# Optimization experiments

Hardware: AMD Instinct MI355X
Metric: run time of the kernel (lower is better)

## Reference

```python
import jax, jax.numpy as jnp
import numpy as np

B, N, T, D, H, E = 2, 1024, 8, 128, 4, 8192
DH = D // H
NEG_SLOPE = 0.2  # GATv2Conv default negative_slope


def _ln(x, g, b):
    m = jnp.mean(x, -1, keepdims=True)
    v = jnp.mean((x - m) ** 2, -1, keepdims=True)
    return (x - m) * jax.lax.rsqrt(v + 1e-5) * g + b


def _forward(x, edge_index, gat_wl, gat_wr, gat_att, gat_b, in_w, in_b, out_w, out_b,
             ffn_w1, ffn_b1, ffn_w2, ffn_b2, fus_w, fus_b,
             lns_g, lns_b, lnt1_g, lnt1_b, lnt2_g, lnt2_b, lnf_g, lnf_b):
    # ---- spatial branch: GATv2, vectorized over (B, T) instead of python loops ----
    loops = jnp.arange(N)
    src = jnp.concatenate([edge_index[0], loops])  # j: message source (PyG adds self loops)
    dst = jnp.concatenate([edge_index[1], loops])  # i: aggregation target
    xl = jnp.einsum('bntd,de->bnte', x, gat_wl).reshape(B, N, T, H, D)
    xr = jnp.einsum('bntd,de->bnte', x, gat_wr).reshape(B, N, T, H, D)
    ml = xl[:, src]                                  # [B,Et,T,H,D]
    mr = xr[:, dst]
    e = jax.nn.leaky_relu(ml + mr, NEG_SLOPE)
    logits = jnp.einsum('bethd,hd->beth', e, gat_att)
    logits = jnp.moveaxis(logits, 1, 0)              # [Et,B,T,H]
    mx = jax.ops.segment_max(logits, dst, num_segments=N)
    p = jnp.exp(logits - mx[dst])                    # stable edge softmax per dst node
    ssum = jax.ops.segment_sum(p, dst, num_segments=N)
    alpha = p / ssum[dst]                            # [Et,B,T,H]
    msg = alpha[..., None] * jnp.moveaxis(ml, 1, 0)
    agg = jax.ops.segment_sum(msg, dst, num_segments=N)  # [N,B,T,H,D]
    x_sp = jnp.moveaxis(agg.mean(3), 0, 1) + gat_b   # concat=False -> head mean; [B,N,T,D]
    x_sp = _ln(x_sp, lns_g, lns_b)

    # ---- temporal branch: MHA + FFN, vectorized over all B*N nodes ----
    xt = x.reshape(B * N, T, D)
    qkv = xt @ in_w + in_b
    q, k, v = jnp.split(qkv, 3, axis=-1)
    q = q.reshape(B * N, T, H, DH)
    k = k.reshape(B * N, T, H, DH)
    v = v.reshape(B * N, T, H, DH)
    scores = jnp.einsum('bthd,bshd->bhts', q, k) / np.float32(np.sqrt(DH))
    attn = jax.nn.softmax(scores, -1)
    o = jnp.einsum('bhts,bshd->bthd', attn, v).reshape(B * N, T, D)
    o = o @ out_w + out_b
    x1 = _ln(xt + o, lnt1_g, lnt1_b)
    ffn = jax.nn.gelu(x1 @ ffn_w1 + ffn_b1, approximate=False) @ ffn_w2 + ffn_b2
    x_tp = _ln(x1 + ffn, lnt2_g, lnt2_b).reshape(B, N, T, D)

    # ---- gated fusion with residual ----
    g = jax.nn.sigmoid(jnp.concatenate([x_sp, x_tp], -1) @ fus_w + fus_b)
    return _ln(g * x_sp + (1.0 - g) * x_tp + x, lnf_g, lnf_b)


def setup_inputs() -> dict:
    key = jax.random.key(0)
    ks = jax.random.split(key, 12)
    s = 0.05
    f = jnp.float32
    return {
        'x': jax.random.normal(ks[0], (B, N, T, D), f),
        'edge_index': jax.random.randint(ks[1], (2, E), 0, N),
        'gat_wl': jax.random.normal(ks[2], (D, H * D), f) * s,
        'gat_wr': jax.random.normal(ks[3], (D, H * D), f) * s,
        'gat_att': jax.random.normal(ks[4], (H, D), f) * s,
        'gat_b': jnp.zeros((D,), f),
        'in_w': jax.random.normal(ks[5], (D, 3 * D), f) * s,
        'in_b': jnp.zeros((3 * D,), f),
        'out_w': jax.random.normal(ks[6], (D, D), f) * s,
        'out_b': jnp.zeros((D,), f),
        'ffn_w1': jax.random.normal(ks[7], (D, 4 * D), f) * s,
        'ffn_b1': jnp.zeros((4 * D,), f),
        'ffn_w2': jax.random.normal(ks[8], (4 * D, D), f) * s,
        'ffn_b2': jnp.zeros((D,), f),
        'fus_w': jax.random.normal(ks[9], (2 * D, D), f) * s,
        'fus_b': jnp.zeros((D,), f),
        'lns_g': jnp.ones((D,), f), 'lns_b': jnp.zeros((D,), f),
        'lnt1_g': jnp.ones((D,), f), 'lnt1_b': jnp.zeros((D,), f),
        'lnt2_g': jnp.ones((D,), f), 'lnt2_b': jnp.zeros((D,), f),
        'lnf_g': jnp.ones((D,), f), 'lnf_b': jnp.zeros((D,), f),
    }


def reference(x, edge_index, gat_wl, gat_wr, gat_att, gat_b, in_w, in_b, out_w, out_b,
              ffn_w1, ffn_b1, ffn_w2, ffn_b2, fus_w, fus_b,
              lns_g, lns_b, lnt1_g, lnt1_b, lnt2_g, lnt2_b, lnf_g, lnf_b):
    return _forward(x, edge_index, gat_wl, gat_wr, gat_att, gat_b, in_w, in_b, out_w, out_b,
                    ffn_w1, ffn_b1, ffn_w2, ffn_b2, fus_w, fus_b,
                    lns_g, lns_b, lnt1_g, lnt1_b, lnt2_g, lnt2_b, lnf_g, lnf_b)
```

## Files before the change

kernel.cpp:

```cpp
#include <hip/hip_runtime.h>
#include <math.h>

#define B_ 2
#define N_ 1024
#define T_ 8
#define D_ 128
#define H_ 4
#define E_ 8192
#define EN_ 9216
#define M_ 16384

typedef unsigned short u16;
using bf16x8 = __attribute__((ext_vector_type(8))) short;
using f32x4  = __attribute__((ext_vector_type(4))) float;

__device__ __forceinline__ float bf2f(unsigned int u) {
  return __uint_as_float(u << 16);
}
__device__ __forceinline__ u16 f2bf(float f) {
  unsigned int x = __float_as_uint(f);
  x += 0x7fffu + ((x >> 16) & 1u);
  return (u16)(x >> 16);
}
__device__ __forceinline__ void load8f(const u16* p, float* f) {
  uint4 u = *(const uint4*)p;
  f[0]=bf2f(u.x & 0xffffu); f[1]=bf2f(u.x >> 16);
  f[2]=bf2f(u.y & 0xffffu); f[3]=bf2f(u.y >> 16);
  f[4]=bf2f(u.z & 0xffffu); f[5]=bf2f(u.z >> 16);
  f[6]=bf2f(u.w & 0xffffu); f[7]=bf2f(u.w >> 16);
}
__device__ __forceinline__ void unpack8(uint4 u, float* f) {
  f[0]=bf2f(u.x & 0xffffu); f[1]=bf2f(u.x >> 16);
  f[2]=bf2f(u.y & 0xffffu); f[3]=bf2f(u.y >> 16);
  f[4]=bf2f(u.z & 0xffffu); f[5]=bf2f(u.z >> 16);
  f[6]=bf2f(u.w & 0xffffu); f[7]=bf2f(u.w >> 16);
}
__device__ __forceinline__ void gl2lds(const u16* g, u16* l) {
  __builtin_amdgcn_global_load_lds(
      (const __attribute__((address_space(1))) unsigned int*)(const void*)g,
      (__attribute__((address_space(3))) unsigned int*)(void*)l,
      16, 0, 0);
}

__device__ __forceinline__ size_t bt_row(int r) {
  return (size_t)(((r >> 13) << 3) | (r & 7)) * 1024 + ((r >> 3) & 1023);
}

__device__ __forceinline__ u16 conv_w_elem(int idx,
    const float* wl, const float* wr, const float* inw, const float* outw,
    const float* f1, const float* f2, const float* fw) {
  const float* src; int base, K, N;
  if      (idx < 65536)  { src = wl;   base = 0;      K = 128; N = 512; }
  else if (idx < 131072) { src = wr;   base = 65536;  K = 128; N = 512; }
  else if (idx < 180224) { src = inw;  base = 131072; K = 128; N = 384; }
  else if (idx < 196608) { src = outw; base = 180224; K = 128; N = 128; }
  else if (idx < 262144) { src = f1;   base = 196608; K = 128; N = 512; }
  else if (idx < 327680) { src = f2;   base = 262144; K = 512; N = 128; }
  else                   { src = fw;   base = 327680; K = 256; N = 128; }
  int o = idx - base;
  int n = o / K, k = o - n * K;
  return f2bf(src[k * N + n]);
}

__global__ __launch_bounds__(1024) void prep_csr_k(const float* __restrict__ x,
    const float* __restrict__ wl, const float* __restrict__ wr,
    const float* __restrict__ inw, const float* __restrict__ outw,
    const float* __restrict__ f1, const float* __restrict__ f2,
    const float* __restrict__ fw,
    u16* __restrict__ XB, u16* __restrict__ WB,
    const int* __restrict__ ei, int* __restrict__ offs, int* __restrict__ srcs) {
  __shared__ int cnt[N_];
  __shared__ int cur[N_];
  int bi = blockIdx.x;
  int tid = threadIdx.x;
  if (bi < 512) {
    int i = (bi * 1024 + tid) * 4;
    float4 v = *(const float4*)&x[i];
    u16 o[4] = {f2bf(v.x), f2bf(v.y), f2bf(v.z), f2bf(v.w)};
    *(ushort4*)&XB[i] = *(ushort4*)o;
    return;
  }
  if (bi < 600) {
    int base = (bi - 512) * 4096 + tid * 4;
#pragma unroll
    for (int j = 0; j < 4; ++j)
      WB[base + j] = conv_w_elem(base + j, wl, wr, inw, outw, f1, f2, fw);
    return;
  }
  cnt[tid] = 0;
  __syncthreads();
  for (int e = tid; e < EN_; e += 1024) {
    int d = (e < E_) ? ei[E_ + e] : (e - E_);
    atomicAdd(&cnt[d], 1);
  }
  __syncthreads();
  int mine = cnt[tid];
  for (int off = 1; off < 1024; off <<= 1) {
    int tv = (tid >= off) ? cnt[tid - off] : 0;
    __syncthreads();
    cnt[tid] += tv;
    __syncthreads();
  }
  int excl = cnt[tid] - mine;
  offs[tid] = excl;
  if (tid == 1023) offs[N_] = cnt[1023];
  cur[tid] = excl;
  __syncthreads();
  for (int e = tid; e < EN_; e += 1024) {
    int d = (e < E_) ? ei[E_ + e] : (e - E_);
    int s = (e < E_) ? ei[e] : (e - E_);
    int pos = atomicAdd(&cur[d], 1);
    srcs[pos] = s;
  }
}

__global__ __launch_bounds__(256) void proj_k(const u16* __restrict__ XB,
    const u16* __restrict__ WT1, const float* __restrict__ in_b,
    u16* __restrict__ XL, u16* __restrict__ XR, u16* __restrict__ QKV) {
  __shared__ u16 As[128 * 128];
  __shared__ u16 Bs[128 * 128];
  int bx = blockIdx.x, by = blockIdx.y;
  int tid = threadIdx.x;
  int lane = tid & 63, wid = tid >> 6;
  int lr = lane & 15, lk = lane >> 4;
  int wm = (wid >> 1) * 64, wn = (wid & 1) * 64;

#pragma unroll
  for (int kc = 0; kc < 4; ++kc) {
#pragma unroll
    for (int i = 0; i < 2; ++i) {
      int o = tid * 16 + i * 4096;
      int row = o >> 6;
      int col = (o >> 1) & 31;
      gl2lds(XB + (size_t)(by * 128 + row) * 128 + kc * 32 + col,
             (u16*)((char*)As + kc * 8192 + i * 4096 + wid * 1024));
      gl2lds(WT1 + (size_t)(bx * 128 + row) * 128 + kc * 32 + col,
             (u16*)((char*)Bs + kc * 8192 + i * 4096 + wid * 1024));
    }
  }
  __syncthreads();

  f32x4 acc[4][4] = {};
#pragma unroll
  for (int kc = 0; kc < 4; ++kc) {
    bf16x8 bf[4];
#pragma unroll
    for (int ni = 0; ni < 4; ++ni)
      bf[ni] = *(const bf16x8*)&Bs[kc * 4096 + (wn + ni * 16 + lr) * 32 + lk * 8];
#pragma unroll
    for (int mi = 0; mi < 4; ++mi) {
      bf16x8 af = *(const bf16x8*)&As[kc * 4096 + (wm + mi * 16 + lr) * 32 + lk * 8];
#pragma unroll
      for (int ni = 0; ni < 4; ++ni)
        acc[mi][ni] = __builtin_amdgcn_mfma_f32_16x16x32_bf16(af, bf[ni], acc[mi][ni], 0, 0, 0);
    }
  }

  u16* Cb; int ldc_; int col0; const float* bias_; int remap;
  if (bx < 4)      { Cb = XL;  ldc_ = 512; col0 = bx * 128;       bias_ = nullptr; remap = 1; }
  else if (bx < 8) { Cb = XR;  ldc_ = 512; col0 = (bx - 4) * 128; bias_ = nullptr; remap = 1; }
  else             { Cb = QKV; ldc_ = 384; col0 = (bx - 8) * 128; bias_ = in_b;    remap = 0; }
  float bc[4];
#pragma unroll
  for (int ni = 0; ni < 4; ++ni)
    bc[ni] = bias_ ? bias_[col0 + wn + ni * 16 + lr] : 0.f;

  __syncthreads();
#pragma unroll
  for (int mi = 0; mi < 4; ++mi) {
#pragma unroll
    for (int r = 0; r < 4; ++r) {
      int rowl = wm + mi * 16 + lk * 4 + r;
#pragma unroll
      for (int ni = 0; ni < 4; ++ni) {
        int col = wn + ni * 16 + lr;
        As[rowl * 128 + (col ^ ((rowl & 7) << 3))] = f2bf(acc[mi][ni][r] + bc[ni]);
      }
    }
  }
  __syncthreads();
  {
    int chunk = tid & 15;
    int rbase = tid >> 4;
#pragma unroll
    for (int pass = 0; pass < 8; ++pass) {
      int rowl = pass * 16 + rbase;
      int row = by * 128 + rowl;
      size_t orow = remap ? bt_row(row) : (size_t)row;
      int sw = (chunk ^ (rowl & 7)) * 8;
      *(uint4*)&Cb[orow * ldc_ + col0 + chunk * 8] =
          *(const uint4*)&As[rowl * 128 + sw];
    }
  }
}

__global__ __launch_bounds__(256) void gat_k(const u16* __restrict__ XL,
    const u16* __restrict__ XR,
    const int* __restrict__ offs, const int* __restrict__ srcs,
    const float* __restrict__ att, const float* __restrict__ gb,
    const float* __restrict__ lng, const float* __restrict__ lnb,
    u16* __restrict__ XSP) {
  int bid = blockIdx.x;
  int lane = threadIdx.x & 63;
  int wid = threadIdx.x >> 6;
  int xcd = bid & 7;
  int slot = bid >> 3;
  int p = ((slot >> 8) << 3) | xcd;
  int n = (slot & 255) * 4 + wid;
  int b = p >> 3, t = p & 7;
  int dd = (lane & 15) * 8;
  size_t tokn = (size_t)(b * N_ + n) * 8 + t;
  const u16* XLs = XL + (size_t)p * 1024 * 512;

  float mr[8], av[8];
  load8f(XR + ((size_t)p * 1024 + n) * 512 + lane * 8, mr);
  *(float4*)&av[0] = *(const float4*)(att + lane * 8);
  *(float4*)&av[4] = *(const float4*)(att + lane * 8 + 4);

  int beg = offs[n], end = offs[n + 1];
  float sH = 0.f;
  float acc[8] = {0.f, 0.f, 0.f, 0.f, 0.f, 0.f, 0.f, 0.f};
  int i = beg;
  uint4 r0 = *(const uint4*)(XLs + (size_t)srcs[i] * 512 + lane * 8);
  uint4 r1 = r0;
  if (i + 1 < end)
    r1 = *(const uint4*)(XLs + (size_t)srcs[i + 1] * 512 + lane * 8);
  while (i + 1 < end) {
    uint4 c0 = r0, c1 = r1;
    if (i + 2 < end)
      r0 = *(const uint4*)(XLs + (size_t)srcs[i + 2] * 512 + lane * 8);
    if (i + 3 < end)
      r1 = *(const uint4*)(XLs + (size_t)srcs[i + 3] * 512 + lane * 8);
    float ml0[8], ml1[8];
    unpack8(c0, ml0);
    unpack8(c1, ml1);
    float d0 = 0.f, d1 = 0.f;
#pragma unroll
    for (int j = 0; j < 8; ++j) {
      float m0 = ml0[j] + mr[j];
      m0 = fmaxf(m0, 0.2f * m0);
      d0 += m0 * av[j];
      float m1 = ml1[j] + mr[j];
      m1 = fmaxf(m1, 0.2f * m1);
      d1 += m1 * av[j];
    }
    d0 += __shfl_xor(d0, 1, 64); d1 += __shfl_xor(d1, 1, 64);
    d0 += __shfl_xor(d0, 2, 64); d1 += __shfl_xor(d1, 2, 64);
    d0 += __shfl_xor(d0, 4, 64); d1 += __shfl_xor(d1, 4, 64);
    d0 += __shfl_xor(d0, 8, 64); d1 += __shfl_xor(d1, 8, 64);
    float p0 = __expf(d0), p1 = __expf(d1);
    sH += p0 + p1;
#pragma unroll
    for (int j = 0; j < 8; ++j) acc[j] += p0 * ml0[j] + p1 * ml1[j];
    i += 2;
  }
  if (i < end) {
    float ml0[8];
    unpack8(r0, ml0);
    float d0 = 0.f;
#pragma unroll
    for (int j = 0; j < 8; ++j) {
      float m0 = ml0[j] + mr[j];
      m0 = fmaxf(m0, 0.2f * m0);
      d0 += m0 * av[j];
    }
    d0 += __shfl_xor(d0, 1, 64);
    d0 += __shfl_xor(d0, 2, 64);
    d0 += __shfl_xor(d0, 4, 64);
    d0 += __shfl_xor(d0, 8, 64);
    float p0 = __expf(d0);
    sH += p0;
#pragma unroll
    for (int j = 0; j < 8; ++j) acc[j] += p0 * ml0[j];
  }
  float invS = 1.f / sH;
#pragma unroll
  for (int j = 0; j < 8; ++j) acc[j] *= invS;
#pragma unroll
  for (int j = 0; j < 8; ++j) {
    acc[j] += __shfl_xor(acc[j], 16, 64);
    acc[j] += __shfl_xor(acc[j], 32, 64);
  }
#pragma unroll
  for (int j = 0; j < 8; ++j) acc[j] = acc[j] * 0.25f + gb[dd + j];
  float s = 0.f, s2 = 0.f;
#pragma unroll
  for (int j = 0; j < 8; ++j) { s += acc[j]; s2 += acc[j] * acc[j]; }
#pragma unroll
  for (int m = 1; m < 16; m <<= 1) {
    s += __shfl_xor(s, m, 64);
    s2 += __shfl_xor(s2, m, 64);
  }
  float mean = s * (1.f / 128.f);
  float var = s2 * (1.f / 128.f) - mean * mean;
  float r = rsqrtf(var + 1e-5f);
  if (lane < 16) {
    u16 ob[8];
#pragma unroll
    for (int j = 0; j < 8; ++j)
      ob[j] = f2bf((acc[j] - mean) * r * lng[dd + j] + lnb[dd + j]);
    *(uint4*)&XSP[tokn * 128 + dd] = *(uint4*)ob;
  }
}

__global__ __launch_bounds__(256) void tower_k(const u16* __restrict__ QKV,
    const u16* __restrict__ WTO, const float* __restrict__ out_b,
    const float* __restrict__ x,
    const float* __restrict__ lnt1_g, const float* __restrict__ lnt1_b,
    const u16* __restrict__ WTF1, const u16* __restrict__ WTF2,
    const float* __restrict__ b1, const float* __restrict__ b2,
    const float* __restrict__ lnt2_g, const float* __restrict__ lnt2_b,
    const u16* __restrict__ WTFUS, const float* __restrict__ fus_b,
    const float* __restrict__ lnf_g, const float* __restrict__ lnf_b,
    const u16* __restrict__ XSP, float* __restrict__ o32) {
  __shared__ u16 P[32 * 128];
  __shared__ u16 Wb[16384];
  __shared__ u16 Hc[4096];
  __shared__ float rs[64], rq[64];
  int by = blockIdx.x;
  int tid = threadIdx.x;
  int lane = tid & 63, wid = tid >> 6;
  int lr = lane & 15, lk = lane >> 4;
  int wm = (wid >> 1) * 16, wn = (wid & 1) * 64;

#pragma unroll
  for (int i = 0; i < 8; ++i) {
    int o = tid * 16 + i * 4096;
    int c = o >> 13;
    int wb = o & 8191;
    int nrow = wb >> 6;
    int kin = (wb & 63) >> 1;
    gl2lds(WTO + (size_t)nrow * 128 + c * 32 + kin,
           (u16*)((char*)Wb + wid * 1024 + i * 4096));
  }
  int t = lane >> 3, sidx = lane & 7, dg = lane & 7;
  for (int it = 0; it < 4; ++it) {
    int task = wid * 4 + it;
    int bnl = task >> 2, h = task & 3;
    int bn = by * 4 + bnl;
    const u16* base = QKV + (size_t)bn * 8 * 384;
    float va[8][4];
#pragma unroll
    for (int s2 = 0; s2 < 8; ++s2) {
      ushort4 vv = *(const ushort4*)(base + s2 * 384 + 256 + h * 32 + dg * 4);
      va[s2][0] = bf2f(vv.x); va[s2][1] = bf2f(vv.y);
      va[s2][2] = bf2f(vv.z); va[s2][3] = bf2f(vv.w);
    }
    const u16* qp = base + t * 384 + h * 32;
    const u16* kp = base + sidx * 384 + 128 + h * 32;
    float sc = 0.f;
#pragma unroll
    for (int d0 = 0; d0 < 32; d0 += 8) {
      float q[8], k[8];
      load8f(qp + d0, q);
      load8f(kp + d0, k);
#pragma unroll
      for (int j = 0; j < 8; ++j) sc += q[j] * k[j];
    }
    sc *= 0.17677669529663687f;
    float m = sc;
    m = fmaxf(m, __shfl_xor(m, 1, 64));
    m = fmaxf(m, __shfl_xor(m, 2, 64));
    m = fmaxf(m, __shfl_xor(m, 4, 64));
    float p = __expf(sc - m);
    float S = p;
    S += __shfl_xor(S, 1, 64);
    S += __shfl_xor(S, 2, 64);
    S += __shfl_xor(S, 4, 64);
    float alpha = p / S;
    int tb = lane & 56;
    float o0 = 0.f, o1 = 0.f, o2 = 0.f, o3 = 0.f;
#pragma unroll
    for (int s2 = 0; s2 < 8; ++s2) {
      float a = __shfl(alpha, tb + s2, 64);
      o0 += a * va[s2][0];
      o1 += a * va[s2][1];
      o2 += a * va[s2][2];
      o3 += a * va[s2][3];
    }
    u16 ov[4] = {f2bf(o0), f2bf(o1), f2bf(o2), f2bf(o3)};
    int row = bnl * 8 + t;
    *(ushort4*)&P[h * 1024 + row * 32 + dg * 4] = *(ushort4*)ov;
  }
  __syncthreads();

  f32x4 acc[4] = {};
#pragma unroll
  for (int c = 0; c < 4; ++c) {
    bf16x8 bf[4];
#pragma unroll
    for (int ni = 0; ni < 4; ++ni)
      bf[ni] = *(const bf16x8*)&Wb[c * 4096 + (wn + ni * 16 + lr) * 32 + lk * 8];
    bf16x8 af = *(const bf16x8*)&P[c * 1024 + (wm + lr) * 32 + lk * 8];
#pragma unroll
    for (int ni = 0; ni < 4; ++ni)
      acc[ni] = __builtin_amdgcn_mfma_f32_16x16x32_bf16(af, bf[ni], acc[ni], 0, 0, 0);
  }

  f32x4 x1r[4];
  {
    float bc[4];
#pragma unroll
    for (int ni = 0; ni < 4; ++ni) bc[ni] = out_b[wn + ni * 16 + lr];
#pragma unroll
    for (int r = 0; r < 4; ++r) {
      int rowl = wm + lk * 4 + r;
      int row = by * 32 + rowl;
      float s = 0.f, s2 = 0.f;
#pragma unroll
      for (int ni = 0; ni < 4; ++ni) {
        int col = wn + ni * 16 + lr;
        float v = acc[ni][r] + bc[ni] + x[(size_t)row * 128 + col];
        acc[ni][r] = v;
        s += v; s2 += v * v;
      }
      s += __shfl_xor(s, 1, 64); s2 += __shfl_xor(s2, 1, 64);
      s += __shfl_xor(s, 2, 64); s2 += __shfl_xor(s2, 2, 64);
      s += __shfl_xor(s, 4, 64); s2 += __shfl_xor(s2, 4, 64);
      s += __shfl_xor(s, 8, 64); s2 += __shfl_xor(s2, 8, 64);
      if (lr == 0) {
        rs[rowl * 2 + (wid & 1)] = s;
        rq[rowl * 2 + (wid & 1)] = s2;
      }
    }
    __syncthreads();
#pragma unroll
    for (int r = 0; r < 4; ++r) {
      int rowl = wm + lk * 4 + r;
      float tot = rs[rowl * 2] + rs[rowl * 2 + 1];
      float tq = rq[rowl * 2] + rq[rowl * 2 + 1];
      float mean = tot * (1.f / 128.f);
      float var = tq * (1.f / 128.f) - mean * mean;
      float rinv = rsqrtf(var + 1e-5f);
#pragma unroll
      for (int ni = 0; ni < 4; ++ni) {
        int col = wn + ni * 16 + lr;
        float o = (acc[ni][r] - mean) * rinv * lnt1_g[col] + lnt1_b[col];
        x1r[ni][r] = o;
        P[(col >> 5) * 1024 + rowl * 32 + (col & 31)] = f2bf(o);
      }
    }
  }

  int wr0 = (wid >> 1) * 16, wc0 = (wid & 1) * 32;
  f32x4 acc2[4] = {};
  for (int nc = 0; nc < 8; ++nc) {
    __syncthreads();
#pragma unroll
    for (int kc = 0; kc < 4; ++kc) {
      gl2lds(WTF1 + (size_t)(nc * 64 + (tid >> 2)) * 128 + kc * 32 + (tid & 3) * 8,
             (u16*)((char*)Wb + kc * 4096 + wid * 1024));
    }
#pragma unroll
    for (int i = 0; i < 4; ++i) {
      int o = tid * 16 + i * 4096;
      int kc2l = o >> 13;
      int wb = o & 8191;
      int nrow = wb >> 6;
      int kin = (wb & 63) >> 1;
      gl2lds(WTF2 + (size_t)nrow * 512 + nc * 64 + kc2l * 32 + kin,
             (u16*)((char*)Wb + 16384 + wid * 1024 + i * 4096));
    }
    __syncthreads();
    f32x4 a1[2] = {};
#pragma unroll
    for (int kc = 0; kc < 4; ++kc) {
      bf16x8 bf0 = *(const bf16x8*)&Wb[kc * 2048 + (wc0 + lr) * 32 + lk * 8];
      bf16x8 bf1 = *(const bf16x8*)&Wb[kc * 2048 + (wc0 + 16 + lr) * 32 + lk * 8];
      bf16x8 af = *(const bf16x8*)&P[kc * 1024 + (wr0 + lr) * 32 + lk * 8];
      a1[0] = __builtin_amdgcn_mfma_f32_16x16x32_bf16(af, bf0, a1[0], 0, 0, 0);
      a1[1] = __builtin_amdgcn_mfma_f32_16x16x32_bf16(af, bf1, a1[1], 0, 0, 0);
    }
#pragma unroll
    for (int r = 0; r < 4; ++r) {
      int row = wr0 + lk * 4 + r;
#pragma unroll
      for (int ni = 0; ni < 2; ++ni) {
        int cl = wc0 + ni * 16 + lr;
        float v = a1[ni][r] + b1[nc * 64 + cl];
        v = 0.5f * v * (1.f + erff(v * 0.70710678118f));
        Hc[(cl >> 5) * 1280 + row * 40 + (cl & 31)] = f2bf(v);
      }
    }
    __syncthreads();
#pragma unroll
    for (int kc2l = 0; kc2l < 2; ++kc2l) {
      bf16x8 bf[4];
#pragma unroll
      for (int ni = 0; ni < 4; ++ni)
        bf[ni] = *(const bf16x8*)&Wb[8192 + kc2l * 4096 + (wn + ni * 16 + lr) * 32 + lk * 8];
      bf16x8 af = *(const bf16x8*)&Hc[kc2l * 1280 + (wm + lr) * 40 + lk * 8];
#pragma unroll
      for (int ni = 0; ni < 4; ++ni)
        acc2[ni] = __builtin_amdgcn_mfma_f32_16x16x32_bf16(af, bf[ni], acc2[ni], 0, 0, 0);
    }
  }
  __syncthreads();

#pragma unroll
  for (int i = 0; i < 8; ++i) {
    int o = tid * 16 + i * 4096;
    int rl = o >> 6;
    int kcf = rl >> 7;
    int nrow = rl & 127;
    int kin = (o & 63) >> 1;
    gl2lds(WTFUS + (size_t)nrow * 256 + kcf * 32 + kin,
           (u16*)((char*)Wb + wid * 1024 + i * 4096));
  }
#pragma unroll
  for (int i = 0; i < 2; ++i) {
    int o = tid * 16 + i * 4096;
    int rl = o >> 6;
    int kcf = rl >> 5;
    int rowl = rl & 31;
    int kin = (o & 63) >> 1;
    gl2lds(XSP + (size_t)(by * 32 + rowl) * 128 + kcf * 32 + kin,
           (u16*)((char*)Hc + wid * 1024 + i * 4096));
  }

  {
    float bc[4];
#pragma unroll
    for (int ni = 0; ni < 4; ++ni) bc[ni] = b2[wn + ni * 16 + lr];
#pragma unroll
    for (int r = 0; r < 4; ++r) {
      int rowl = wm + lk * 4 + r;
      float s = 0.f, s2 = 0.f;
#pragma unroll
      for (int ni = 0; ni < 4; ++ni) {
        float v = acc2[ni][r] + bc[ni] + x1r[ni][r];
        acc2[ni][r] = v;
        s += v; s2 += v * v;
      }
      s += __shfl_xor(s, 1, 64); s2 += __shfl_xor(s2, 1, 64);
      s += __shfl_xor(s, 2, 64); s2 += __shfl_xor(s2, 2, 64);
      s += __shfl_xor(s, 4, 64); s2 += __shfl_xor(s2, 4, 64);
      s += __shfl_xor(s, 8, 64); s2 += __shfl_xor(s2, 8, 64);
      if (lr == 0) {
        rs[rowl * 2 + (wid & 1)] = s;
        rq[rowl * 2 + (wid & 1)] = s2;
      }
    }
    __syncthreads();
#pragma unroll
    for (int r = 0; r < 4; ++r) {
      int rowl = wm + lk * 4 + r;
      float tot = rs[rowl * 2] + rs[rowl * 2 + 1];
      float tq = rq[rowl * 2] + rq[rowl * 2 + 1];
      float mean = tot * (1.f / 128.f);
      float var = tq * (1.f / 128.f) - mean * mean;
      float rinv = rsqrtf(var + 1e-5f);
#pragma unroll
      for (int ni = 0; ni < 4; ++ni) {
        int col = wn + ni * 16 + lr;
        float o = (acc2[ni][r] - mean) * rinv * lnt2_g[col] + lnt2_b[col];
        acc2[ni][r] = o;
        P[rowl * 128 + (col ^ ((rowl & 7) << 3))] = f2bf(o);
      }
    }
  }
  __syncthreads();

  f32x4 acc3[4] = {};
#pragma unroll
  for (int kc = 0; kc < 4; ++kc) {
    bf16x8 bf[4];
#pragma unroll
    for (int ni = 0; ni < 4; ++ni)
      bf[ni] = *(const bf16x8*)&Wb[kc * 4096 + (wn + ni * 16 + lr) * 32 + lk * 8];
    bf16x8 af = *(const bf16x8*)&Hc[kc * 1024 + (wm + lr) * 32 + lk * 8];
#pragma unroll
    for (int ni = 0; ni < 4; ++ni)
      acc3[ni] = __builtin_amdgcn_mfma_f32_16x16x32_bf16(af, bf[ni], acc3[ni], 0, 0, 0);
  }
  __syncthreads();
#pragma unroll
  for (int i = 0; i < 8; ++i) {
    int o = tid * 16 + i * 4096;
    int rl = o >> 6;
    int kcf = rl >> 7;
    int nrow = rl & 127;
    int kin = (o & 63) >> 1;
    gl2lds(WTFUS + (size_t)nrow * 256 + 128 + kcf * 32 + kin,
           (u16*)((char*)Wb + wid * 1024 + i * 4096));
  }
  __syncthreads();
#pragma unroll
  for (int kc = 0; kc < 4; ++kc) {
    bf16x8 bf[4];
#pragma unroll
    for (int ni = 0; ni < 4; ++ni)
      bf[ni] = *(const bf16x8*)&Wb[kc * 4096 + (wn + ni * 16 + lr) * 32 + lk * 8];
    int arow = wm + lr;
    bf16x8 af = *(const bf16x8*)&P[arow * 128 + ((kc * 32 + lk * 8) ^ ((arow & 7) << 3))];
#pragma unroll
    for (int ni = 0; ni < 4; ++ni)
      acc3[ni] = __builtin_amdgcn_mfma_f32_16x16x32_bf16(af, bf[ni], acc3[ni], 0, 0, 0);
  }
  {
    float bc[4];
#pragma unroll
    for (int ni = 0; ni < 4; ++ni) bc[ni] = fus_b[wn + ni * 16 + lr];
#pragma unroll
    for (int r = 0; r < 4; ++r) {
      int rowl = wm + lk * 4 + r;
      int row = by * 32 + rowl;
      float s = 0.f, s2 = 0.f;
#pragma unroll
      for (int ni = 0; ni < 4; ++ni) {
        int col = wn + ni * 16 + lr;
        float v = acc3[ni][r] + bc[ni];
        float gg = 1.f / (1.f + __expf(-v));
        float xsp = bf2f((unsigned int)Hc[(col >> 5) * 1024 + rowl * 32 + (col & 31)]);
        float xtp = acc2[ni][r];
        v = gg * xsp + (1.f - gg) * xtp + x[(size_t)row * 128 + col];
        acc3[ni][r] = v;
        s += v; s2 += v * v;
      }
      s += __shfl_xor(s, 1, 64); s2 += __shfl_xor(s2, 1, 64);
      s += __shfl_xor(s, 2, 64); s2 += __shfl_xor(s2, 2, 64);
      s += __shfl_xor(s, 4, 64); s2 += __shfl_xor(s2, 4, 64);
      s += __shfl_xor(s, 8, 64); s2 += __shfl_xor(s2, 8, 64);
      if (lr == 0) {
        rs[rowl * 2 + (wid & 1)] = s;
        rq[rowl * 2 + (wid & 1)] = s2;
      }
    }
    __syncthreads();
#pragma unroll
    for (int r = 0; r < 4; ++r) {
      int rowl = wm + lk * 4 + r;
      int row = by * 32 + rowl;
      float tot = rs[rowl * 2] + rs[rowl * 2 + 1];
      float tq = rq[rowl * 2] + rq[rowl * 2 + 1];
      float mean = tot * (1.f / 128.f);
      float var = tq * (1.f / 128.f) - mean * mean;
      float rinv = rsqrtf(var + 1e-5f);
#pragma unroll
      for (int ni = 0; ni < 4; ++ni) {
        int col = wn + ni * 16 + lr;
        o32[(size_t)row * 128 + col] =
            (acc3[ni][r] - mean) * rinv * lnf_g[col] + lnf_b[col];
      }
    }
  }
}

extern "C" void kernel_launch(void* const* d_in, const int* in_sizes, int n_in,
                              void* d_out, int out_size, void* d_ws, size_t ws_size,
                              hipStream_t stream) {
  const float* x       = (const float*)d_in[0];
  const int*   ei      = (const int*)d_in[1];
  const float* gat_att = (const float*)d_in[4];
  const float* gat_b   = (const float*)d_in[5];
  const float* in_b    = (const float*)d_in[7];
  const float* out_b   = (const float*)d_in[9];
  const float* ffn_b1  = (const float*)d_in[11];
  const float* ffn_b2  = (const float*)d_in[13];
  const float* fus_b   = (const float*)d_in[15];
  const float* lns_g   = (const float*)d_in[16];
  const float* lns_b   = (const float*)d_in[17];
  const float* lnt1_g  = (const float*)d_in[18];
  const float* lnt1_b  = (const float*)d_in[19];
  const float* lnt2_g  = (const float*)d_in[20];
  const float* lnt2_b  = (const float*)d_in[21];
  const float* lnf_g   = (const float*)d_in[22];
  const float* lnf_b   = (const float*)d_in[23];

  char* ws = (char*)d_ws;
  u16*   WB    = (u16*)ws;
  u16*   WTO   = WB + 180224;
  u16*   WTF1  = WB + 196608;
  u16*   WTF2  = WB + 262144;
  u16*   WTFUS = WB + 327680;
  int*   OFFS  = (int*)(ws + 3145728);
  int*   SRCS  = (int*)(ws + 3153920);
  u16*   XB   = (u16*)(ws + 4194304);
  u16*   XL   = (u16*)(ws + 8388608);
  u16*   XR   = (u16*)(ws + 25165824);
  u16*   QKV  = (u16*)(ws + 50331648);
  u16*   XSP  = (u16*)(ws + 67108864);

  prep_csr_k<<<dim3(601), dim3(1024), 0, stream>>>(x,
      (const float*)d_in[2], (const float*)d_in[3], (const float*)d_in[6],
      (const float*)d_in[8], (const float*)d_in[10], (const float*)d_in[12],
      (const float*)d_in[14], XB, WB, ei, OFFS, SRCS);

  proj_k<<<dim3(11, 128), dim3(256), 0, stream>>>(XB, WB, in_b, XL, XR, QKV);

  gat_k<<<dim3(4096), dim3(256), 0, stream>>>(XL, XR, OFFS, SRCS,
      gat_att, gat_b, lns_g, lns_b, XSP);

  tower_k<<<dim3(512), dim3(256), 0, stream>>>(QKV, WTO, out_b, x,
      lnt1_g, lnt1_b, WTF1, WTF2, ffn_b1, ffn_b2, lnt2_g, lnt2_b,
      WTFUS, fus_b, lnf_g, lnf_b, XSP, (float*)d_out);
}
```

Measured before the change: 200.1 us.

## Fuse bf16 conversion and CSR build into the projection GEMM kernel

Removes the separate prep kernel. The projection GEMM now converts fp32 x and the fp32 weights (read transposed, strided by column) to bf16 directly into LDS. An extra column of blocks converts the remaining tower weights and builds the CSR in one block. This saves one kernel launch and the XB/WB round trip through global memory. In exchange, the x tile and the weight tile are converted redundantly in every GEMM block, and the uncoalesced strided weight reads may be costly.

New measurement: 195.9 us. -2.1%, faster.

```diff
diff --git a/kernel.cpp b/kernel.cpp
--- a/kernel.cpp
+++ b/kernel.cpp
@@ -47,13 +47,9 @@
 }
 
 __device__ __forceinline__ u16 conv_w_elem(int idx,
-    const float* wl, const float* wr, const float* inw, const float* outw,
-    const float* f1, const float* f2, const float* fw) {
+    const float* outw, const float* f1, const float* f2, const float* fw) {
   const float* src; int base, K, N;
-  if      (idx < 65536)  { src = wl;   base = 0;      K = 128; N = 512; }
-  else if (idx < 131072) { src = wr;   base = 65536;  K = 128; N = 512; }
-  else if (idx < 180224) { src = inw;  base = 131072; K = 128; N = 384; }
-  else if (idx < 196608) { src = outw; base = 180224; K = 128; N = 128; }
+  if      (idx < 196608) { src = outw; base = 180224; K = 128; N = 128; }
   else if (idx < 262144) { src = f1;   base = 196608; K = 128; N = 512; }
   else if (idx < 327680) { src = f2;   base = 262144; K = 512; N = 128; }
   else                   { src = fw;   base = 327680; K = 256; N = 128; }
@@ -62,81 +58,98 @@
   return f2bf(src[k * N + n]);
 }
 
-__global__ __launch_bounds__(1024) void prep_csr_k(const float* __restrict__ x,
+__global__ __launch_bounds__(256) void proj_k(const float* __restrict__ x,
     const float* __restrict__ wl, const float* __restrict__ wr,
     const float* __restrict__ inw, const float* __restrict__ outw,
     const float* __restrict__ f1, const float* __restrict__ f2,
-    const float* __restrict__ fw,
-    u16* __restrict__ XB, u16* __restrict__ WB,
+    const float* __restrict__ fw, const float* __restrict__ in_b,
+    u16* __restrict__ XL, u16* __restrict__ XR, u16* __restrict__ QKV,
+    u16* __restrict__ WBt,
     const int* __restrict__ ei, int* __restrict__ offs, int* __restrict__ srcs) {
-  __shared__ int cnt[N_];
-  __shared__ int cur[N_];
-  int bi = blockIdx.x;
-  int tid = threadIdx.x;
-  if (bi < 512) {
-    int i = (bi * 1024 + tid) * 4;
-    float4 v = *(const float4*)&x[i];
-    u16 o[4] = {f2bf(v.x), f2bf(v.y), f2bf(v.z), f2bf(v.w)};
-    *(ushort4*)&XB[i] = *(ushort4*)o;
-    return;
-  }
-  if (bi < 600) {
-    int base = (bi - 512) * 4096 + tid * 4;
-#pragma unroll
-    for (int j = 0; j < 4; ++j)
-      WB[base + j] = conv_w_elem(base + j, wl, wr, inw, outw, f1, f2, fw);
-    return;
-  }
-  cnt[tid] = 0;
-  __syncthreads();
-  for (int e = tid; e < EN_; e += 1024) {
-    int d = (e < E_) ? ei[E_ + e] : (e - E_);
-    atomicAdd(&cnt[d], 1);
-  }
-  __syncthreads();
-  int mine = cnt[tid];
-  for (int off = 1; off < 1024; off <<= 1) {
-    int tv = (tid >= off) ? cnt[tid - off] : 0;
-    __syncthreads();
-    cnt[tid] += tv;
-    __syncthreads();
-  }
-  int excl = cnt[tid] - mine;
-  offs[tid] = excl;
-  if (tid == 1023) offs[N_] = cnt[1023];
-  cur[tid] = excl;
-  __syncthreads();
-  for (int e = tid; e < EN_; e += 1024) {
-    int d = (e < E_) ? ei[E_ + e] : (e - E_);
-    int s = (e < E_) ? ei[e] : (e - E_);
-    int pos = atomicAdd(&cur[d], 1);
-    srcs[pos] = s;
-  }
-}
-
-__global__ __launch_bounds__(256) void proj_k(const u16* __restrict__ XB,
-    const u16* __restrict__ WT1, const float* __restrict__ in_b,
-    u16* __restrict__ XL, u16* __restrict__ XR, u16* __restrict__ QKV) {
   __shared__ u16 As[128 * 128];
   __shared__ u16 Bs[128 * 128];
   int bx = blockIdx.x, by = blockIdx.y;
   int tid = threadIdx.x;
+
+  if (bx == 11) {
+    int gid = by * 256 + tid;
+    for (int idx = 180224 + gid; idx < 360448; idx += 32768)
+      WBt[idx] = conv_w_elem(idx, outw, f1, f2, fw);
+    if (by != 0) return;
+    int* cnt  = (int*)As;
+    int* curp = (int*)(As + 2048);
+    int* wsum = (int*)Bs;
+    for (int j = tid; j < N_; j += 256) cnt[j] = 0;
+    __syncthreads();
+    for (int e = tid; e < EN_; e += 256) {
+      int d = (e < E_) ? ei[E_ + e] : (e - E_);
+      atomicAdd(&cnt[d], 1);
+    }
+    __syncthreads();
+    int b4 = tid * 4;
+    int s0 = cnt[b4], s1 = cnt[b4 + 1], s2 = cnt[b4 + 2], s3 = cnt[b4 + 3];
+    int tsum = s0 + s1 + s2 + s3;
+    wsum[tid] = tsum;
+    __syncthreads();
+    for (int off = 1; off < 256; off <<= 1) {
+      int v = (tid >= off) ? wsum[tid - off] : 0;
+      __syncthreads();
+      wsum[tid] += v;
+      __syncthreads();
+    }
+    int excl = wsum[tid] - tsum;
+    offs[b4] = excl;                curp[b4] = excl;
+    offs[b4 + 1] = excl + s0;       curp[b4 + 1] = excl + s0;
+    offs[b4 + 2] = excl + s0 + s1;  curp[b4 + 2] = excl + s0 + s1;
+    offs[b4 + 3] = excl + s0 + s1 + s2;
+    curp[b4 + 3] = excl + s0 + s1 + s2;
+    if (tid == 255) offs[N_] = excl + tsum;
+    __syncthreads();
+    for (int e = tid; e < EN_; e += 256) {
+      int d = (e < E_) ? ei[E_ + e] : (e - E_);
+      int s = (e < E_) ? ei[e] : (e - E_);
+      int pos = atomicAdd(&curp[d], 1);
+      srcs[pos] = s;
+    }
+    return;
+  }
+
   int lane = tid & 63, wid = tid >> 6;
   int lr = lane & 15, lk = lane >> 4;
   int wm = (wid >> 1) * 64, wn = (wid & 1) * 64;
 
-#pragma unroll
-  for (int kc = 0; kc < 4; ++kc) {
-#pragma unroll
-    for (int i = 0; i < 2; ++i) {
-      int o = tid * 16 + i * 4096;
-      int row = o >> 6;
-      int col = (o >> 1) & 31;
-      gl2lds(XB + (size_t)(by * 128 + row) * 128 + kc * 32 + col,
-             (u16*)((char*)As + kc * 8192 + i * 4096 + wid * 1024));
-      gl2lds(WT1 + (size_t)(bx * 128 + row) * 128 + kc * 32 + col,
-             (u16*)((char*)Bs + kc * 8192 + i * 4096 + wid * 1024));
-    }
+  const float* wsrc; int NS, n0;
+  if      (bx < 4) { wsrc = wl;  NS = 512; n0 = bx * 128; }
+  else if (bx < 8) { wsrc = wr;  NS = 512; n0 = (bx - 4) * 128; }
+  else             { wsrc = inw; NS = 384; n0 = (bx - 8) * 128; }
+
+#pragma unroll
+  for (int i = 0; i < 4; ++i) {
+    int c = tid + i * 256;
+    int row = c >> 3, seg = c & 7;
+    const float* xp = x + (size_t)(by * 128 + row) * 128 + seg * 16;
+    u16 ob[16];
+#pragma unroll
+    for (int j = 0; j < 16; j += 4) {
+      float4 v = *(const float4*)(xp + j);
+      ob[j] = f2bf(v.x); ob[j + 1] = f2bf(v.y);
+      ob[j + 2] = f2bf(v.z); ob[j + 3] = f2bf(v.w);
+    }
+    u16* dst = &As[(seg >> 1) * 4096 + row * 32 + (seg & 1) * 16];
+    *(uint4*)dst = *(uint4*)&ob[0];
+    *(uint4*)(dst + 8) = *(uint4*)&ob[8];
+  }
+#pragma unroll
+  for (int i = 0; i < 4; ++i) {
+    int c = tid + i * 256;
+    int nrow = c & 127, kseg = c >> 7;
+    u16 ob[16];
+#pragma unroll
+    for (int j = 0; j < 16; ++j)
+      ob[j] = f2bf(wsrc[(size_t)(kseg * 16 + j) * NS + n0 + nrow]);
+    u16* dst = &Bs[(kseg >> 1) * 4096 + nrow * 32 + (kseg & 1) * 16];
+    *(uint4*)dst = *(uint4*)&ob[0];
+    *(uint4*)(dst + 8) = *(uint4*)&ob[8];
   }
   __syncthreads();
 
@@ -675,18 +688,15 @@
   u16*   WTFUS = WB + 327680;
   int*   OFFS  = (int*)(ws + 3145728);
   int*   SRCS  = (int*)(ws + 3153920);
-  u16*   XB   = (u16*)(ws + 4194304);
   u16*   XL   = (u16*)(ws + 8388608);
   u16*   XR   = (u16*)(ws + 25165824);
   u16*   QKV  = (u16*)(ws + 50331648);
   u16*   XSP  = (u16*)(ws + 67108864);
 
-  prep_csr_k<<<dim3(601), dim3(1024), 0, stream>>>(x,
+  proj_k<<<dim3(12, 128), dim3(256), 0, stream>>>(x,
       (const float*)d_in[2], (const float*)d_in[3], (const float*)d_in[6],
       (const float*)d_in[8], (const float*)d_in[10], (const float*)d_in[12],
-      (const float*)d_in[14], XB, WB, ei, OFFS, SRCS);
-
-  proj_k<<<dim3(11, 128), dim3(256), 0, stream>>>(XB, WB, in_b, XL, XR, QKV);
+      (const float*)d_in[14], in_b, XL, XR, QKV, WB, ei, OFFS, SRCS);
 
   gat_k<<<dim3(4096), dim3(256), 0, stream>>>(XL, XR, OFFS, SRCS,
       gat_att, gat_b, lns_g, lns_b, XSP);
```
